# Optimization experiments

Hardware: AMD Instinct MI355X
Metric: run time of the kernel (lower is better)

Reference implementation:

```python
import jax, jax.numpy as jnp
import numpy as np
from jax import lax

TTQ_THRESHOLD_FACTOR = 0.05


def ttq_quantize(w, wp, wn, t):
    # w: [O,I,k,k]; wp, wn: [1] (already abs'ed); t: scalar threshold
    mask_pos = w > t
    mask_neg = w < -t
    return mask_pos.astype(w.dtype) * wp[0] - mask_neg.astype(w.dtype) * wn[0]


def setup_inputs() -> dict:
    key = jax.random.key(0)
    k1, k2, k3 = jax.random.split(key, 3)
    B, Cin, H, W = 64, 128, 56, 56
    Cout, K = 256, 3
    x = jax.random.normal(k1, (B, Cin, H, W), dtype=jnp.float32)
    # kaiming-uniform-ish init scale; exact init distribution does not matter for math
    weight = jax.random.normal(k2, (Cout, Cin, K, K), dtype=jnp.float32) * 0.05
    bias = jax.random.normal(k3, (Cout,), dtype=jnp.float32) * 0.01
    wp = jnp.full((1,), 0.1, dtype=jnp.float32)
    wn = jnp.full((1,), 0.1, dtype=jnp.float32)
    return {"x": x, "weight": weight, "bias": bias, "wp": wp, "wn": wn}


def reference(x, weight, bias, wp, wn):
    # threshold computed on detached weight
    t = TTQ_THRESHOLD_FACTOR * jnp.max(jnp.abs(lax.stop_gradient(weight)))
    qw = ttq_quantize(weight, jnp.abs(wp), jnp.abs(wn), t)
    out = lax.conv_general_dilated(
        x, qw,
        window_strides=(1, 1), padding="VALID",
        dimension_numbers=("NCHW", "OIHW", "NCHW"),
    )
    return out + bias[None, :, None, None]
```

## Files before the change

### kernel.cpp

```cpp
#include <hip/hip_runtime.h>
#include <hip/hip_bf16.h>

#define BATCH 64
#define CIN   128
#define HIN   56
#define WIN   56
#define COUT  256
#define KSZ   3
#define OHP   54
#define OWP   54
#define NSPAT (OHP * OWP)
#define NTILES 23
#define KDIM  (CIN * KSZ * KSZ)

typedef short bf16x8 __attribute__((ext_vector_type(8)));
typedef float f32x4  __attribute__((ext_vector_type(4)));

static __device__ __forceinline__ unsigned short f2bf(float f) {
    unsigned v = __float_as_uint(f);
    v += 0x7FFFu + ((v >> 16) & 1u);
    return (unsigned short)(v >> 16);
}

static __device__ __forceinline__ void gl_lds16(const void* g, void* l) {
    __builtin_amdgcn_global_load_lds(
        (const __attribute__((address_space(1))) void*)g,
        (__attribute__((address_space(3))) void*)l, 16, 0, 0);
}

__global__ __launch_bounds__(256) void maxabs_kernel(const float* __restrict__ w,
                                                     float* __restrict__ blockmax, int n) {
    float m = 0.f;
    for (int i = blockIdx.x * 256 + threadIdx.x; i < n; i += gridDim.x * 256)
        m = fmaxf(m, fabsf(w[i]));
    for (int off = 32; off > 0; off >>= 1)
        m = fmaxf(m, __shfl_down(m, off));
    __shared__ float red[4];
    if ((threadIdx.x & 63) == 0) red[threadIdx.x >> 6] = m;
    __syncthreads();
    if (threadIdx.x == 0)
        blockmax[blockIdx.x] = fmaxf(fmaxf(red[0], red[1]), fmaxf(red[2], red[3]));
}

__global__ __launch_bounds__(256) void quant_kernel(const float* __restrict__ w,
                                                    const float* __restrict__ wp,
                                                    const float* __restrict__ wn,
                                                    const float* __restrict__ blockmax,
                                                    unsigned short* __restrict__ qw) {
    __shared__ float red[4];
    float m = blockmax[threadIdx.x];
    for (int off = 32; off > 0; off >>= 1)
        m = fmaxf(m, __shfl_down(m, off));
    if ((threadIdx.x & 63) == 0) red[threadIdx.x >> 6] = m;
    __syncthreads();
    float t = 0.05f * fmaxf(fmaxf(red[0], red[1]), fmaxf(red[2], red[3]));

    int idx = blockIdx.x * 256 + threadIdx.x;
    float p = fabsf(wp[0]), nn = fabsf(wn[0]);
    float v = w[idx];
    float q = (v > t) ? p : ((v < -t) ? -nn : 0.0f);
    int co  = idx / KDIM;
    int rem = idx - co * KDIM;
    int ci  = rem / 9;
    int kk  = rem - ci * 9;
    qw[co * KDIM + kk * CIN + ci] = f2bf(q);
}

__global__ __launch_bounds__(256) void cast_nhwc_kernel(const float* __restrict__ x,
                                                        unsigned* __restrict__ xt_u32) {
    int b = blockIdx.x / HIN;
    int h = blockIdx.x - b * HIN;
    __shared__ float xs[CIN][57];
#pragma unroll
    for (int it = 0; it < 7; ++it) {
        int id = it * 256 + threadIdx.x;
        int ci = id / 14;
        int wq = (id - ci * 14) * 4;
        float4 v = *(const float4*)(x + (((size_t)(b * CIN + ci)) * HIN + h) * WIN + wq);
        xs[ci][wq + 0] = v.x; xs[ci][wq + 1] = v.y;
        xs[ci][wq + 2] = v.z; xs[ci][wq + 3] = v.w;
    }
    __syncthreads();
#pragma unroll
    for (int it = 0; it < 7; ++it) {
        int id = it * 256 + threadIdx.x;
        int w_ = id >> 5;
        int cq = (id & 31) * 4;
        unsigned u0 = (unsigned)f2bf(xs[cq + 0][w_]) | ((unsigned)f2bf(xs[cq + 1][w_]) << 16);
        unsigned u1 = (unsigned)f2bf(xs[cq + 2][w_]) | ((unsigned)f2bf(xs[cq + 3][w_]) << 16);
        uint2 val; val.x = u0; val.y = u1;
        *(uint2*)&xt_u32[((size_t)(b * HIN + h) * WIN + w_) * 64 + (id & 31) * 2] = val;
    }
}

__global__ __launch_bounds__(256, 3) void conv_mfma_kernel(const unsigned short* __restrict__ xt,
                                                           const unsigned short* __restrict__ qw,
                                                           const float* __restrict__ bias,
                                                           float* __restrict__ out) {
    int xcd = blockIdx.x & 7;
    int k   = blockIdx.x >> 3;
    int g   = k / 46;
    int r   = k - g * 46;
    int b   = g * 8 + xcd;
    int mt  = r / 23;
    int nt  = r - mt * 23;

    __shared__ __align__(16) unsigned short As[128 * 64];
    __shared__ __align__(16) unsigned short Bs[128 * 64];

    int t    = threadIdx.x;
    int wave = t >> 6, lane = t & 63;
    int wm   = wave >> 1, wcol = wave & 1;
    int quad = lane >> 4, r16 = lane & 15;

    int row0 = t >> 3;
    int lc   = (t & 7) ^ (row0 & 7);

    const unsigned short* Ab = qw + (size_t)(mt * 128 + row0) * KDIM + lc * 8;
    const unsigned short* Bb[4];
#pragma unroll
    for (int c = 0; c < 4; ++c) {
        unsigned n = nt * 128 + c * 32 + row0;
        if (n > NSPAT - 1) n = NSPAT - 1;
        unsigned oh = n / OWP, ow = n - oh * OWP;
        Bb[c] = xt + ((size_t)(b * HIN + oh) * WIN + ow) * CIN + lc * 8;
    }

    f32x4 acc[4][4] = {};

#pragma unroll
    for (int kk = 0; kk < 18; ++kk) {
        int slice = kk >> 1;
        int kh = slice / 3, kw = slice - kh * 3;
        int boff = (kh * WIN + kw) * CIN + (kk & 1) * 64;
        int aoff = kk * 64;

#pragma unroll
        for (int c = 0; c < 4; ++c) {
            gl_lds16(Ab + aoff + c * 32 * KDIM, (char*)As + c * 4096 + wave * 1024);
            gl_lds16(Bb[c] + boff,              (char*)Bs + c * 4096 + wave * 1024);
        }
        __syncthreads();

#pragma unroll
        for (int s = 0; s < 2; ++s) {
            int pc = ((s * 4 + quad) ^ (r16 & 7)) * 8;
            bf16x8 af[4], bfr[4];
#pragma unroll
            for (int i = 0; i < 4; ++i)
                af[i] = *(const bf16x8*)&As[(wm * 64 + i * 16 + r16) * 64 + pc];
#pragma unroll
            for (int j = 0; j < 4; ++j)
                bfr[j] = *(const bf16x8*)&Bs[(wcol * 64 + j * 16 + r16) * 64 + pc];
#pragma unroll
            for (int i = 0; i < 4; ++i)
#pragma unroll
                for (int j = 0; j < 4; ++j)
                    acc[i][j] = __builtin_amdgcn_mfma_f32_16x16x32_bf16(af[i], bfr[j], acc[i][j], 0, 0, 0);
        }
        __syncthreads();
    }

#pragma unroll
    for (int i = 0; i < 4; ++i) {
        int co_base = mt * 128 + wm * 64 + i * 16 + quad * 4;
        float4 bv = *(const float4*)(bias + co_base);
#pragma unroll
        for (int j = 0; j < 4; ++j) {
            unsigned n = nt * 128 + wcol * 64 + j * 16 + r16;
            if (n < NSPAT) {
                out[(size_t)(b * COUT + co_base + 0) * NSPAT + n] = acc[i][j][0] + bv.x;
                out[(size_t)(b * COUT + co_base + 1) * NSPAT + n] = acc[i][j][1] + bv.y;
                out[(size_t)(b * COUT + co_base + 2) * NSPAT + n] = acc[i][j][2] + bv.z;
                out[(size_t)(b * COUT + co_base + 3) * NSPAT + n] = acc[i][j][3] + bv.w;
            }
        }
    }
}

extern "C" void kernel_launch(void* const* d_in, const int* in_sizes, int n_in,
                              void* d_out, int out_size, void* d_ws, size_t ws_size,
                              hipStream_t stream) {
    const float* x      = (const float*)d_in[0];
    const float* weight = (const float*)d_in[1];
    const float* bias   = (const float*)d_in[2];
    const float* wp     = (const float*)d_in[3];
    const float* wn     = (const float*)d_in[4];
    float* out          = (float*)d_out;

    float*          bmax = (float*)d_ws;
    unsigned short* qw   = (unsigned short*)((char*)d_ws + 1024);
    unsigned short* xt   = (unsigned short*)((char*)d_ws + 590848);

    maxabs_kernel<<<256, 256, 0, stream>>>(weight, bmax, COUT * KDIM);
    quant_kernel<<<(COUT * KDIM) / 256, 256, 0, stream>>>(weight, wp, wn, bmax, qw);
    cast_nhwc_kernel<<<BATCH * HIN, 256, 0, stream>>>(x, (unsigned*)xt);
    conv_mfma_kernel<<<2 * BATCH * NTILES, 256, 0, stream>>>(xt, qw, bias, out);
}
```

Baseline: 386.7 us.

## Double-buffer conv GEMM with 256x256 tiles over flattened batch-spatial dim

The conv kernel becomes a 512-thread, 256(Cout)x256(flattened batch*spatial) tile GEMM. It double-buffers LDS, interleaving global-to-LDS loads of the next K slice with MFMA on the current one, using explicit waitcnt, barriers and setprio. Flattening N across the batch removes the padded partial spatial tiles, and the quant and NHWC cast kernels are merged into one launch. The cost is higher register and LDS pressure, with one block per tile covering all output channels.

```diff
diff --git a/kernel.cpp b/kernel.cpp
--- a/kernel.cpp
+++ b/kernel.cpp
@@ -1,5 +1,4 @@
 #include <hip/hip_runtime.h>
-#include <hip/hip_bf16.h>
 
 #define BATCH 64
 #define CIN   128
@@ -10,8 +9,11 @@
 #define OHP   54
 #define OWP   54
 #define NSPAT (OHP * OWP)
-#define NTILES 23
+#define NFLAT (BATCH * NSPAT)
 #define KDIM  (CIN * KSZ * KSZ)
+#define NBLK  (NFLAT / 256)
+#define NCAST (BATCH * HIN)
+#define NQNT  ((COUT * KDIM) / 256)
 
 typedef short bf16x8 __attribute__((ext_vector_type(8)));
 typedef float f32x4  __attribute__((ext_vector_type(4)));
@@ -27,6 +29,12 @@
         (const __attribute__((address_space(1))) void*)g,
         (__attribute__((address_space(3))) void*)l, 16, 0, 0);
 }
+
+#define BAR()   asm volatile("s_barrier" ::: "memory")
+#define LGKM0() asm volatile("s_waitcnt lgkmcnt(0)" ::: "memory")
+#define VMC2()  asm volatile("s_waitcnt vmcnt(2)" ::: "memory")
+#define VMC0()  asm volatile("s_waitcnt vmcnt(0)" ::: "memory")
+#define SB0()   __builtin_amdgcn_sched_barrier(0)
 
 __global__ __launch_bounds__(256) void maxabs_kernel(const float* __restrict__ w,
                                                      float* __restrict__ blockmax, int n) {
@@ -42,138 +50,199 @@
         blockmax[blockIdx.x] = fmaxf(fmaxf(red[0], red[1]), fmaxf(red[2], red[3]));
 }
 
-__global__ __launch_bounds__(256) void quant_kernel(const float* __restrict__ w,
-                                                    const float* __restrict__ wp,
-                                                    const float* __restrict__ wn,
-                                                    const float* __restrict__ blockmax,
-                                                    unsigned short* __restrict__ qw) {
-    __shared__ float red[4];
-    float m = blockmax[threadIdx.x];
-    for (int off = 32; off > 0; off >>= 1)
-        m = fmaxf(m, __shfl_down(m, off));
-    if ((threadIdx.x & 63) == 0) red[threadIdx.x >> 6] = m;
-    __syncthreads();
-    float t = 0.05f * fmaxf(fmaxf(red[0], red[1]), fmaxf(red[2], red[3]));
-
-    int idx = blockIdx.x * 256 + threadIdx.x;
-    float p = fabsf(wp[0]), nn = fabsf(wn[0]);
-    float v = w[idx];
-    float q = (v > t) ? p : ((v < -t) ? -nn : 0.0f);
-    int co  = idx / KDIM;
-    int rem = idx - co * KDIM;
-    int ci  = rem / 9;
-    int kk  = rem - ci * 9;
-    qw[co * KDIM + kk * CIN + ci] = f2bf(q);
-}
-
-__global__ __launch_bounds__(256) void cast_nhwc_kernel(const float* __restrict__ x,
-                                                        unsigned* __restrict__ xt_u32) {
-    int b = blockIdx.x / HIN;
-    int h = blockIdx.x - b * HIN;
-    __shared__ float xs[CIN][57];
-#pragma unroll
-    for (int it = 0; it < 7; ++it) {
-        int id = it * 256 + threadIdx.x;
-        int ci = id / 14;
-        int wq = (id - ci * 14) * 4;
-        float4 v = *(const float4*)(x + (((size_t)(b * CIN + ci)) * HIN + h) * WIN + wq);
-        xs[ci][wq + 0] = v.x; xs[ci][wq + 1] = v.y;
-        xs[ci][wq + 2] = v.z; xs[ci][wq + 3] = v.w;
-    }
-    __syncthreads();
-#pragma unroll
-    for (int it = 0; it < 7; ++it) {
-        int id = it * 256 + threadIdx.x;
-        int w_ = id >> 5;
-        int cq = (id & 31) * 4;
-        unsigned u0 = (unsigned)f2bf(xs[cq + 0][w_]) | ((unsigned)f2bf(xs[cq + 1][w_]) << 16);
-        unsigned u1 = (unsigned)f2bf(xs[cq + 2][w_]) | ((unsigned)f2bf(xs[cq + 3][w_]) << 16);
-        uint2 val; val.x = u0; val.y = u1;
-        *(uint2*)&xt_u32[((size_t)(b * HIN + h) * WIN + w_) * 64 + (id & 31) * 2] = val;
-    }
-}
-
-__global__ __launch_bounds__(256, 3) void conv_mfma_kernel(const unsigned short* __restrict__ xt,
+__global__ __launch_bounds__(256) void prep_kernel(const float* __restrict__ x,
+                                                   const float* __restrict__ w,
+                                                   const float* __restrict__ wp,
+                                                   const float* __restrict__ wn,
+                                                   const float* __restrict__ blockmax,
+                                                   unsigned short* __restrict__ qw,
+                                                   unsigned* __restrict__ xt_u32) {
+    int bid = blockIdx.x;
+    if (bid < NCAST) {
+        int b = bid / HIN;
+        int h = bid - b * HIN;
+        __shared__ float xs[CIN][57];
+#pragma unroll
+        for (int it = 0; it < 7; ++it) {
+            int id = it * 256 + threadIdx.x;
+            int ci = id / 14;
+            int wq = (id - ci * 14) * 4;
+            float4 v = *(const float4*)(x + (((size_t)(b * CIN + ci)) * HIN + h) * WIN + wq);
+            xs[ci][wq + 0] = v.x; xs[ci][wq + 1] = v.y;
+            xs[ci][wq + 2] = v.z; xs[ci][wq + 3] = v.w;
+        }
+        __syncthreads();
+#pragma unroll
+        for (int it = 0; it < 7; ++it) {
+            int id = it * 256 + threadIdx.x;
+            int w_ = id >> 5;
+            int cq = (id & 31) * 4;
+            unsigned u0 = (unsigned)f2bf(xs[cq + 0][w_]) | ((unsigned)f2bf(xs[cq + 1][w_]) << 16);
+            unsigned u1 = (unsigned)f2bf(xs[cq + 2][w_]) | ((unsigned)f2bf(xs[cq + 3][w_]) << 16);
+            uint2 val; val.x = u0; val.y = u1;
+            *(uint2*)&xt_u32[((size_t)(b * HIN + h) * WIN + w_) * 64 + (id & 31) * 2] = val;
+        }
+    } else {
+        __shared__ float red[4];
+        float m = blockmax[threadIdx.x];
+        for (int off = 32; off > 0; off >>= 1)
+            m = fmaxf(m, __shfl_down(m, off));
+        if ((threadIdx.x & 63) == 0) red[threadIdx.x >> 6] = m;
+        __syncthreads();
+        float t = 0.05f * fmaxf(fmaxf(red[0], red[1]), fmaxf(red[2], red[3]));
+
+        int idx = (bid - NCAST) * 256 + threadIdx.x;
+        float p = fabsf(wp[0]), nn = fabsf(wn[0]);
+        float v = w[idx];
+        float qv = (v > t) ? p : ((v < -t) ? -nn : 0.0f);
+        int co  = idx / KDIM;
+        int rem = idx - co * KDIM;
+        int ci  = rem / 9;
+        int kk  = rem - ci * 9;
+        qw[co * KDIM + kk * CIN + ci] = f2bf(qv);
+    }
+}
+
+__global__ __launch_bounds__(512, 2) void conv_mfma_kernel(const unsigned short* __restrict__ xt,
                                                            const unsigned short* __restrict__ qw,
                                                            const float* __restrict__ bias,
                                                            float* __restrict__ out) {
-    int xcd = blockIdx.x & 7;
-    int k   = blockIdx.x >> 3;
-    int g   = k / 46;
-    int r   = k - g * 46;
-    int b   = g * 8 + xcd;
-    int mt  = r / 23;
-    int nt  = r - mt * 23;
-
-    __shared__ __align__(16) unsigned short As[128 * 64];
-    __shared__ __align__(16) unsigned short Bs[128 * 64];
-
-    int t    = threadIdx.x;
-    int wave = t >> 6, lane = t & 63;
-    int wm   = wave >> 1, wcol = wave & 1;
-    int quad = lane >> 4, r16 = lane & 15;
-
-    int row0 = t >> 3;
-    int lc   = (t & 7) ^ (row0 & 7);
-
-    const unsigned short* Ab = qw + (size_t)(mt * 128 + row0) * KDIM + lc * 8;
-    const unsigned short* Bb[4];
+    unsigned orig = blockIdx.x;
+    unsigned xcd = orig & 7u, loc = orig >> 3;
+    const unsigned q91 = NBLK / 8u, r1 = NBLK % 8u;
+    unsigned wgid = (xcd < r1 ? xcd * (q91 + 1) : r1 * (q91 + 1) + (xcd - r1) * q91) + loc;
+    unsigned n0 = wgid * 256u;
+
+    __shared__ __align__(16) unsigned short sm[2][32768];
+
+    const int tid   = threadIdx.x;
+    const int wave  = tid >> 6, lane = tid & 63;
+    const int wrow  = wave >> 2;
+    const int wcol  = wave & 3;
+    const int quad  = lane >> 4, r16 = lane & 15;
+    const int row_s = tid >> 3;
+    const int lc    = (tid & 7) ^ (row_s & 7);
+
+    const unsigned short* Ag = qw + (size_t)row_s * KDIM + lc * 8;
+    const unsigned short* Bg[4];
 #pragma unroll
     for (int c = 0; c < 4; ++c) {
-        unsigned n = nt * 128 + c * 32 + row0;
-        if (n > NSPAT - 1) n = NSPAT - 1;
-        unsigned oh = n / OWP, ow = n - oh * OWP;
-        Bb[c] = xt + ((size_t)(b * HIN + oh) * WIN + ow) * CIN + lc * 8;
-    }
-
-    f32x4 acc[4][4] = {};
-
-#pragma unroll
-    for (int kk = 0; kk < 18; ++kk) {
-        int slice = kk >> 1;
-        int kh = slice / 3, kw = slice - kh * 3;
-        int boff = (kh * WIN + kw) * CIN + (kk & 1) * 64;
-        int aoff = kk * 64;
-
-#pragma unroll
-        for (int c = 0; c < 4; ++c) {
-            gl_lds16(Ab + aoff + c * 32 * KDIM, (char*)As + c * 4096 + wave * 1024);
-            gl_lds16(Bb[c] + boff,              (char*)Bs + c * 4096 + wave * 1024);
-        }
-        __syncthreads();
-
-#pragma unroll
-        for (int s = 0; s < 2; ++s) {
-            int pc = ((s * 4 + quad) ^ (r16 & 7)) * 8;
-            bf16x8 af[4], bfr[4];
-#pragma unroll
-            for (int i = 0; i < 4; ++i)
-                af[i] = *(const bf16x8*)&As[(wm * 64 + i * 16 + r16) * 64 + pc];
-#pragma unroll
-            for (int j = 0; j < 4; ++j)
-                bfr[j] = *(const bf16x8*)&Bs[(wcol * 64 + j * 16 + r16) * 64 + pc];
-#pragma unroll
-            for (int i = 0; i < 4; ++i)
-#pragma unroll
-                for (int j = 0; j < 4; ++j)
-                    acc[i][j] = __builtin_amdgcn_mfma_f32_16x16x32_bf16(af[i], bfr[j], acc[i][j], 0, 0, 0);
-        }
-        __syncthreads();
-    }
-
-#pragma unroll
-    for (int i = 0; i < 4; ++i) {
-        int co_base = mt * 128 + wm * 64 + i * 16 + quad * 4;
-        float4 bv = *(const float4*)(bias + co_base);
-#pragma unroll
-        for (int j = 0; j < 4; ++j) {
-            unsigned n = nt * 128 + wcol * 64 + j * 16 + r16;
-            if (n < NSPAT) {
-                out[(size_t)(b * COUT + co_base + 0) * NSPAT + n] = acc[i][j][0] + bv.x;
-                out[(size_t)(b * COUT + co_base + 1) * NSPAT + n] = acc[i][j][1] + bv.y;
-                out[(size_t)(b * COUT + co_base + 2) * NSPAT + n] = acc[i][j][2] + bv.z;
-                out[(size_t)(b * COUT + co_base + 3) * NSPAT + n] = acc[i][j][3] + bv.w;
-            }
+        unsigned n = n0 + c * 64 + row_s;
+        unsigned b = n / NSPAT, rem = n - b * NSPAT;
+        unsigned oh = rem / OWP, ow = rem - oh * OWP;
+        Bg[c] = xt + ((size_t)((b * HIN + oh) * WIN + ow)) * CIN + lc * 8;
+    }
+
+    auto stA = [&](int slot, int c, int kt) {
+        gl_lds16(Ag + (size_t)c * (64 * KDIM) + kt * 64,
+                 (char*)sm + slot * 65536 + c * 8192 + wave * 1024);
+    };
+    auto stB = [&](int slot, int c, int boff) {
+        gl_lds16(Bg[c] + boff,
+                 (char*)sm + slot * 65536 + 32768 + c * 8192 + wave * 1024);
+    };
+
+    f32x4 acc[8][4] = {};
+
+    const int pc0 = (quad ^ (r16 & 7)) * 8;
+    const int pc1 = ((4 + quad) ^ (r16 & 7)) * 8;
+    const int ar  = wrow * 128 + r16;
+    const int br  = wcol * 64  + r16;
+
+#define MROW(I, AF) \
+    acc[I][0] = __builtin_amdgcn_mfma_f32_16x16x32_bf16(AF, bfr0, acc[I][0], 0, 0, 0); \
+    acc[I][1] = __builtin_amdgcn_mfma_f32_16x16x32_bf16(AF, bfr1, acc[I][1], 0, 0, 0); \
+    acc[I][2] = __builtin_amdgcn_mfma_f32_16x16x32_bf16(AF, bfr2, acc[I][2], 0, 0, 0); \
+    acc[I][3] = __builtin_amdgcn_mfma_f32_16x16x32_bf16(AF, bfr3, acc[I][3], 0, 0, 0);
+
+    {
+        stB(0, 0, 0); stB(0, 1, 0); stB(0, 2, 0); stB(0, 3, 0);
+        stA(0, 0, 0); stA(0, 2, 0); stA(0, 1, 0); stA(0, 3, 0);
+        VMC2(); BAR();
+    }
+
+#pragma unroll
+    for (int t = 0; t < 18; ++t) {
+        const int cur = t & 1, nxt = cur ^ 1;
+        const int t1  = t + 1;
+        const int sl1 = t1 >> 1;
+        const int kh1 = sl1 / 3, kw1 = sl1 - 3 * (sl1 / 3);
+        const int boff1 = (kh1 * WIN + kw1) * CIN + (t1 & 1) * 64;
+        const unsigned short* Ac = &sm[cur][0];
+        const unsigned short* Bc = &sm[cur][16384];
+
+        bf16x8 af0, af1, af2, af3, bfr0, bfr1, bfr2, bfr3;
+
+        af0  = *(const bf16x8*)&Ac[(ar +  0) * 64 + pc0];
+        af1  = *(const bf16x8*)&Ac[(ar + 16) * 64 + pc0];
+        af2  = *(const bf16x8*)&Ac[(ar + 32) * 64 + pc0];
+        af3  = *(const bf16x8*)&Ac[(ar + 48) * 64 + pc0];
+        bfr0 = *(const bf16x8*)&Bc[(br +  0) * 64 + pc0];
+        bfr1 = *(const bf16x8*)&Bc[(br + 16) * 64 + pc0];
+        bfr2 = *(const bf16x8*)&Bc[(br + 32) * 64 + pc0];
+        bfr3 = *(const bf16x8*)&Bc[(br + 48) * 64 + pc0];
+        if (t < 17) { stB(nxt, 0, boff1); stB(nxt, 1, boff1); }
+        BAR(); LGKM0(); SB0();
+        __builtin_amdgcn_s_setprio(1);
+        MROW(0, af0) MROW(1, af1) MROW(2, af2) MROW(3, af3)
+        __builtin_amdgcn_s_setprio(0); SB0();
+        if (t < 17) { VMC2(); } else { VMC0(); }
+        BAR();
+
+        af0 = *(const bf16x8*)&Ac[(ar +  64) * 64 + pc0];
+        af1 = *(const bf16x8*)&Ac[(ar +  80) * 64 + pc0];
+        af2 = *(const bf16x8*)&Ac[(ar +  96) * 64 + pc0];
+        af3 = *(const bf16x8*)&Ac[(ar + 112) * 64 + pc0];
+        if (t < 17) { stB(nxt, 2, boff1); stB(nxt, 3, boff1); }
+        BAR(); LGKM0(); SB0();
+        __builtin_amdgcn_s_setprio(1);
+        MROW(4, af0) MROW(5, af1) MROW(6, af2) MROW(7, af3)
+        __builtin_amdgcn_s_setprio(0); SB0();
+        BAR();
+
+        af0  = *(const bf16x8*)&Ac[(ar +  0) * 64 + pc1];
+        af1  = *(const bf16x8*)&Ac[(ar + 16) * 64 + pc1];
+        af2  = *(const bf16x8*)&Ac[(ar + 32) * 64 + pc1];
+        af3  = *(const bf16x8*)&Ac[(ar + 48) * 64 + pc1];
+        bfr0 = *(const bf16x8*)&Bc[(br +  0) * 64 + pc1];
+        bfr1 = *(const bf16x8*)&Bc[(br + 16) * 64 + pc1];
+        bfr2 = *(const bf16x8*)&Bc[(br + 32) * 64 + pc1];
+        bfr3 = *(const bf16x8*)&Bc[(br + 48) * 64 + pc1];
+        if (t < 17) { stA(nxt, 0, t1); stA(nxt, 2, t1); }
+        BAR(); LGKM0(); SB0();
+        __builtin_amdgcn_s_setprio(1);
+        MROW(0, af0) MROW(1, af1) MROW(2, af2) MROW(3, af3)
+        __builtin_amdgcn_s_setprio(0); SB0();
+        BAR();
+
+        af0 = *(const bf16x8*)&Ac[(ar +  64) * 64 + pc1];
+        af1 = *(const bf16x8*)&Ac[(ar +  80) * 64 + pc1];
+        af2 = *(const bf16x8*)&Ac[(ar +  96) * 64 + pc1];
+        af3 = *(const bf16x8*)&Ac[(ar + 112) * 64 + pc1];
+        if (t < 17) { stA(nxt, 1, t1); stA(nxt, 3, t1); }
+        BAR(); LGKM0(); SB0();
+        __builtin_amdgcn_s_setprio(1);
+        MROW(4, af0) MROW(5, af1) MROW(6, af2) MROW(7, af3)
+        __builtin_amdgcn_s_setprio(0); SB0();
+        if (t < 17) { VMC2(); }
+        BAR();
+    }
+#undef MROW
+
+#pragma unroll
+    for (int j = 0; j < 4; ++j) {
+        unsigned n = n0 + wcol * 64 + j * 16 + r16;
+        unsigned b = n / NSPAT, rem = n - b * NSPAT;
+        size_t ob = (size_t)b * COUT * NSPAT + rem;
+#pragma unroll
+        for (int i = 0; i < 8; ++i) {
+            int co = wrow * 128 + i * 16 + quad * 4;
+            float4 bv = *(const float4*)(bias + co);
+            size_t o = ob + (size_t)co * NSPAT;
+            out[o]             = acc[i][j][0] + bv.x;
+            out[o + NSPAT]     = acc[i][j][1] + bv.y;
+            out[o + 2 * NSPAT] = acc[i][j][2] + bv.z;
+            out[o + 3 * NSPAT] = acc[i][j][3] + bv.w;
         }
     }
 }
@@ -193,7 +262,6 @@
     unsigned short* xt   = (unsigned short*)((char*)d_ws + 590848);
 
     maxabs_kernel<<<256, 256, 0, stream>>>(weight, bmax, COUT * KDIM);
-    quant_kernel<<<(COUT * KDIM) / 256, 256, 0, stream>>>(weight, wp, wn, bmax, qw);
-    cast_nhwc_kernel<<<BATCH * HIN, 256, 0, stream>>>(x, (unsigned*)xt);
-    conv_mfma_kernel<<<2 * BATCH * NTILES, 256, 0, stream>>>(xt, qw, bias, out);
-}
+    prep_kernel<<<NCAST + NQNT, 256, 0, stream>>>(x, weight, wp, wn, bmax, qw, (unsigned*)xt);
+    conv_mfma_kernel<<<NBLK, 512, 0, stream>>>(xt, qw, bias, out);
+}
```

New measurement: 454.8 us. 1.18x slower.
